# Performance work log

Measured on AMD Instinct MI355X. Metric: run time of the kernel, lower is better.

The kernel has to match this reference:

```python
import jax, jax.numpy as jnp
import numpy as np

B, S, HID = 2, 2048, 4096
NH, D = 32, 128          # heads, head_dim
G, GS = 8, 4             # palu groups, group_size (heads per group)
RK = 256                 # rank per K group (rank_k[i])
RV = 2048                # total V rank
FGD = RV // G            # fused_group_dim = 256
FH = FGD * NH            # fused_hidden_dim = 8192
GD = HID // G            # k group_dim = 512
THETA = 10000.0


def setup_inputs() -> dict:
    key = jax.random.key(0)
    ks = jax.random.split(key, 7)
    hidden_states = jax.random.normal(ks[0], (B, S, HID), jnp.float32)
    causal = jnp.tril(jnp.ones((S, S), bool))
    attention_mask = jnp.broadcast_to(
        jnp.where(causal, 0.0, -1e9).astype(jnp.float32)[None, None], (B, 1, S, S))
    position_ids = jnp.broadcast_to(jnp.arange(S, dtype=jnp.int32)[None], (B, S))
    sc = 0.02
    Wq = sc * jax.random.normal(ks[1], (HID, HID), jnp.float32)
    WVT = sc * jax.random.normal(ks[2], (G * RK, HID), jnp.float32)   # k_proj.VT
    U = sc * jax.random.normal(ks[3], (GD, G * RK), jnp.float32)      # k_proj.U
    Wv = sc * jax.random.normal(ks[4], (RV, HID), jnp.float32)
    Wo = sc * jax.random.normal(ks[5], (HID, FH), jnp.float32)
    return dict(hidden_states=hidden_states, attention_mask=attention_mask,
                position_ids=position_ids, Wq=Wq, WVT=WVT, U=U, Wv=Wv, Wo=Wo)


def _rotate_half(x):
    return jnp.concatenate([-x[..., D // 2:], x[..., :D // 2]], axis=-1)


def reference(hidden_states, attention_mask, position_ids, Wq, WVT, U, Wv, Wo):
    b, q, _ = hidden_states.shape
    # projections
    qs = (hidden_states @ Wq.T).reshape(b, q, NH, D).transpose(0, 2, 1, 3)      # (b,H,q,d)
    k_lat = (hidden_states @ WVT.T).reshape(b, q, G, RK).transpose(0, 2, 1, 3)  # (b,G,q,RK)
    v_lat = (hidden_states @ Wv.T).reshape(b, q, G, FGD).transpose(0, 2, 1, 3)  # (b,G,q,FGD)
    # headwise reconstruction of K: group g latent (RK) -> group_dim (512) via U[:, g-slice]
    Ug = U.reshape(GD, G, RK)
    keys = jnp.einsum('bgsr,dgr->bgsd', k_lat, Ug)                 # (b,G,q,512)
    keys = keys.transpose(0, 2, 1, 3).reshape(b, q, NH, D).transpose(0, 2, 1, 3)  # (b,H,q,d)
    # RoPE
    inv_freq = 1.0 / (THETA ** (jnp.arange(0, D, 2, dtype=jnp.float32) / D))
    freqs = position_ids.astype(jnp.float32)[..., None] * inv_freq            # (b,q,d/2)
    emb = jnp.concatenate([freqs, freqs], axis=-1)
    cos, sin = jnp.cos(emb)[:, None], jnp.sin(emb)[:, None]                   # (b,1,q,d)
    qs = qs * cos + _rotate_half(qs) * sin
    keys = keys * cos + _rotate_half(keys) * sin
    # attention scores + mask + fp32 softmax
    attn = jnp.einsum('bhqd,bhkd->bhqk', qs, keys) / np.sqrt(D).astype(np.float32)
    attn = attn + attention_mask
    attn = jax.nn.softmax(attn.astype(jnp.float32), axis=-1).astype(qs.dtype)
    # PALU fused low-rank V path: exact torch reshape/transpose semantics
    aw = attn.reshape(b, G, q * GS, q)                                        # (b,G,gs*q,kv)
    out = jnp.einsum('bgik,bgkf->bgif', aw, v_lat)                            # (b,G,gs*q,FGD)
    out = out.transpose(0, 2, 1, 3).reshape(b, q, FH)                         # (b,q,8192)
    return out @ Wo.T
```

## Files before the change

kernel.cpp:

```cpp
#include <hip/hip_runtime.h>
#include <hip/hip_bf16.h>

typedef __hip_bfloat16 bf16;
typedef __bf16 bf16x8 __attribute__((ext_vector_type(8)));
typedef float f32x4 __attribute__((ext_vector_type(4)));

#define MFMA16(a, b, c) __builtin_amdgcn_mfma_f32_16x16x32_bf16(a, b, c, 0, 0, 0)

__device__ __forceinline__ void llds16(const bf16* g, bf16* lds) {
  __builtin_amdgcn_global_load_lds(
      (const __attribute__((address_space(1))) unsigned int*)g,
      (__attribute__((address_space(3))) unsigned int*)lds, 16, 0, 0);
}

__device__ __forceinline__ void storeC(float* p, float v) { *p = v; }
__device__ __forceinline__ void storeC(bf16* p, float v) { *p = __float2bfloat16(v); }

__global__ __launch_bounds__(256) void cvt_f2b(const float* __restrict__ in,
                                               bf16* __restrict__ out, int n4) {
  int i = blockIdx.x * 256 + threadIdx.x;
  if (i >= n4) return;
  float4 v = ((const float4*)in)[i];
  union { bf16 h[4]; short4 s; } u;
  u.h[0] = __float2bfloat16(v.x);
  u.h[1] = __float2bfloat16(v.y);
  u.h[2] = __float2bfloat16(v.z);
  u.h[3] = __float2bfloat16(v.w);
  ((short4*)out)[i] = u.s;
}

template <typename OUT_T>
__global__ __launch_bounds__(512, 2) void gemm256(
    const bf16* __restrict__ A, const bf16* __restrict__ B, OUT_T* __restrict__ C,
    int K, int lda, int ldb, int ldc) {
  extern __shared__ bf16 sm[];
  const int t = threadIdx.x, w = t >> 6, l = t & 63;
  const int lane_r = l & 15, quad = l >> 4;
  const int wm = (w >> 2) * 128, wn = (w & 3) * 64;
  const long m0 = (long)blockIdx.y * 256, n0 = (long)blockIdx.x * 256;
  const int r0 = t >> 2;
  const int c0 = (((t & 3) ^ (r0 & 3)) << 3);
  const bf16* As0 = A + (m0 + r0) * lda + c0;
  const bf16* As1 = A + (m0 + r0 + 128) * lda + c0;
  const bf16* Bs0 = B + (n0 + r0) * ldb + c0;
  const bf16* Bs1 = B + (n0 + r0 + 128) * ldb + c0;

#define STAGE(sl, kt)                                   \
  do {                                                  \
    long ko = (long)(kt) * 32;                          \
    bf16* dA = sm + (sl) * 16384;                       \
    bf16* dB = dA + 8192;                               \
    llds16(As0 + ko, dA + t * 8);                       \
    llds16(As1 + ko, dA + (t + 512) * 8);               \
    llds16(Bs0 + ko, dB + t * 8);                       \
    llds16(Bs1 + ko, dB + (t + 512) * 8);               \
  } while (0)

  f32x4 acc[8][4] = {};
  const int KT = K >> 5;
  const int sw = quad ^ (lane_r & 3);

  STAGE(0, 0);
  STAGE(1, 1);
  int sl = 0;
  for (int kt = 0; kt < KT; ++kt) {
    const int pre = KT - 1 - kt;
    if (pre >= 2) {
      int sl2 = sl + 2;
      if (sl2 >= 3) sl2 -= 3;
      STAGE(sl2, kt + 2);
      asm volatile("s_waitcnt vmcnt(8)" ::: "memory");
    } else if (pre == 1) {
      asm volatile("s_waitcnt vmcnt(4)" ::: "memory");
    } else {
      asm volatile("s_waitcnt vmcnt(0)" ::: "memory");
    }
    __builtin_amdgcn_s_barrier();
    __builtin_amdgcn_sched_barrier(0);
    const bf16* Al = sm + sl * 16384;
    const bf16* Bl = Al + 8192;
    bf16x8 af[8], bfr[4];
#pragma unroll
    for (int mt = 0; mt < 8; ++mt)
      af[mt] = *(const bf16x8*)&Al[(wm + mt * 16 + lane_r) * 32 + sw * 8];
#pragma unroll
    for (int nt = 0; nt < 4; ++nt)
      bfr[nt] = *(const bf16x8*)&Bl[(wn + nt * 16 + lane_r) * 32 + sw * 8];
    __builtin_amdgcn_s_setprio(1);
#pragma unroll
    for (int mt = 0; mt < 8; ++mt)
#pragma unroll
      for (int nt = 0; nt < 4; ++nt)
        acc[mt][nt] = MFMA16(af[mt], bfr[nt], acc[mt][nt]);
    __builtin_amdgcn_s_setprio(0);
    __builtin_amdgcn_s_barrier();
    if (++sl == 3) sl = 0;
  }
#undef STAGE

#pragma unroll
  for (int mt = 0; mt < 8; ++mt)
#pragma unroll
    for (int nt = 0; nt < 4; ++nt) {
      long row = m0 + wm + mt * 16 + quad * 4;
      long col = n0 + wn + nt * 16 + lane_r;
#pragma unroll
      for (int r = 0; r < 4; ++r) storeC(&C[(row + r) * ldc + col], acc[mt][nt][r]);
    }
}

template <typename OUT_T>
__global__ __launch_bounds__(256) void gemm_bt(
    const bf16* __restrict__ A, const bf16* __restrict__ B, OUT_T* __restrict__ C,
    int M, int N, int K, int lda, int ldb, int ldc,
    long batchA, long batchB, long batchC) {
  __shared__ alignas(16) bf16 As[128 * 32];
  __shared__ alignas(16) bf16 Bs[128 * 32];
  const int t = threadIdx.x;
  const int w = t >> 6, l = t & 63;
  const int lane_r = l & 15, quad = l >> 4;
  const int wm = (w >> 1) * 64, wn = (w & 1) * 64;
  const long m0 = (long)blockIdx.y * 128, n0 = (long)blockIdx.x * 128;
  A += (long)blockIdx.z * batchA;
  B += (long)blockIdx.z * batchB;
  C += (long)blockIdx.z * batchC;
  const int r0a = t >> 2;
  const int cba = (t & 3) * 8;
  f32x4 acc[4][4] = {};
  for (int k0 = 0; k0 < K; k0 += 32) {
    llds16(A + (m0 + r0a) * lda + k0 + cba, &As[t * 8]);
    llds16(A + (m0 + r0a + 64) * lda + k0 + cba, &As[(t + 256) * 8]);
    llds16(B + (n0 + r0a) * ldb + k0 + cba, &Bs[t * 8]);
    llds16(B + (n0 + r0a + 64) * ldb + k0 + cba, &Bs[(t + 256) * 8]);
    __syncthreads();
    bf16x8 af[4], bfr[4];
#pragma unroll
    for (int mt = 0; mt < 4; ++mt)
      af[mt] = *(const bf16x8*)&As[(wm + mt * 16 + lane_r) * 32 + quad * 8];
#pragma unroll
    for (int nt = 0; nt < 4; ++nt)
      bfr[nt] = *(const bf16x8*)&Bs[(wn + nt * 16 + lane_r) * 32 + quad * 8];
#pragma unroll
    for (int mt = 0; mt < 4; ++mt)
#pragma unroll
      for (int nt = 0; nt < 4; ++nt)
        acc[mt][nt] = MFMA16(af[mt], bfr[nt], acc[mt][nt]);
    __syncthreads();
  }
#pragma unroll
  for (int mt = 0; mt < 4; ++mt)
#pragma unroll
    for (int nt = 0; nt < 4; ++nt) {
      long row = m0 + wm + mt * 16 + quad * 4;
      long col = n0 + wn + nt * 16 + lane_r;
#pragma unroll
      for (int r = 0; r < 4; ++r) storeC(&C[(row + r) * ldc + col], acc[mt][nt][r]);
    }
}

__global__ __launch_bounds__(256) void rope_perm(const bf16* __restrict__ in, int ldin,
                                                 bf16* __restrict__ out,
                                                 const int* __restrict__ pos_ids) {
  int idx = blockIdx.x * 256 + threadIdx.x;
  int d = idx & 63;
  int h = (idx >> 6) & 31;
  int bs = idx >> 11;
  int b = bs >> 11, s = bs & 2047;
  float pos = (float)pos_ids[bs];
  float inv = exp2f(-(float)d * (13.287712379549449f / 64.0f));
  float fr = pos * inv, sn, cs;
  sincosf(fr, &sn, &cs);
  long bi = (long)bs * ldin + h * 128 + d;
  long bo = ((long)(b * 32 + h) * 2048 + s) * 128 + d;
  float x1 = __bfloat162float(in[bi]);
  float x2 = __bfloat162float(in[bi + 64]);
  out[bo] = __float2bfloat16(x1 * cs - x2 * sn);
  out[bo + 64] = __float2bfloat16(x2 * cs + x1 * sn);
}

__global__ __launch_bounds__(256) void transpose_kernel(const bf16* __restrict__ v,
                                                        int ldv,
                                                        bf16* __restrict__ vt) {
  __shared__ bf16 tile[32][33];
  int b = blockIdx.z;
  int c0 = blockIdx.x * 32;
  int r0 = blockIdx.y * 32;
  int tx = threadIdx.x & 31, ty = threadIdx.x >> 5;
#pragma unroll
  for (int p = 0; p < 4; ++p) {
    int r = ty + p * 8;
    tile[r][tx] = v[((long)b * 2048 + r0 + r) * ldv + c0 + tx];
  }
  __syncthreads();
#pragma unroll
  for (int p = 0; p < 4; ++p) {
    int cidx = ty + p * 8;
    int cg = c0 + cidx;
    int g = cg >> 8, d = cg & 255;
    int s = r0 + tx;
    vt[((long)((b * 8 + g) * 64 + (s >> 5))) * 8192 + d * 32 + (s & 31)] = tile[tx][cidx];
  }
}

__global__ __launch_bounds__(512, 2) void attn_kernel(const bf16* __restrict__ Q,
                                                      const bf16* __restrict__ Kg,
                                                      const bf16* __restrict__ Vt,
                                                      bf16* __restrict__ fused) {
  __shared__ alignas(16) bf16 smem[32768];
  const int t = threadIdx.x, w = t >> 6, l = t & 63;
  const int lane_r = l & 15, quad = l >> 4;
  const int L = blockIdx.x;
  const int half = L >> 8, pair = L & 255;
  const int hb = pair >> 2, slot = pair & 3;
  const int qt = half ? slot : (7 - slot);
  const int b = hb >> 5, h = hb & 31;
  const int g = h >> 2, j = h & 3;
  const int q0 = qt * 256;
  const int qr0 = q0 + w * 32;
  const float scale = 0.08838834764831845f;

  const bf16* qbase = Q + ((long)(b * 32 + h) * 2048 + qr0 + lane_r) * 128 + quad * 8;
  bf16x8 qf[2][4];
#pragma unroll
  for (int m = 0; m < 2; ++m)
#pragma unroll
    for (int kd = 0; kd < 4; ++kd)
      qf[m][kd] = *(const bf16x8*)(qbase + m * 2048 + kd * 32);

  f32x4 acc[2][16] = {};
  float m_i[2][4], l_i[2][4];
#pragma unroll
  for (int m = 0; m < 2; ++m)
#pragma unroll
    for (int r = 0; r < 4; ++r) { m_i[m][r] = -1e30f; l_i[m][r] = 0.f; }

  const bf16* Kf = Kg + (long)(b * 32 + h) * 262144 + lane_r * 128 + quad * 8;
  const bf16* Vf = Vt + (long)(b * 8 + g) * 524288 + lane_r * 32 + quad * 8;
  bf16* Pw = smem + w * 1024;
  const int pslot = quad ^ ((lane_r >> 1) & 3);
  int poff0[4], poff1[4];
  {
    const int hi = lane_r >> 3, lo = lane_r & 7;
#pragma unroll
    for (int r = 0; r < 4; ++r) {
      int rq = quad * 4 + r;
      int sw = (rq >> 1) & 3;
      poff0[r] = rq * 32 + ((hi ^ sw) << 3) + lo;
      poff1[r] = rq * 32 + (((2 + hi) ^ sw) << 3) + lo;
    }
  }

  const int nkw = (qr0 >> 5) + 1;
  for (int kt = 0; kt < nkw; ++kt) {
    const int k0 = kt * 32;
    const bool diag = (kt == nkw - 1);
    const bf16* Kt_ = Kf + (long)k0 * 128;
    const bf16* Vt_ = Vf + (long)kt * 8192;

    f32x4 s[2][2] = {};
#pragma unroll
    for (int ks = 0; ks < 2; ++ks) {
      bf16x8 kf[4];
#pragma unroll
      for (int kd = 0; kd < 4; ++kd)
        kf[kd] = *(const bf16x8*)(Kt_ + ks * 2048 + kd * 32);
#pragma unroll
      for (int kd = 0; kd < 4; ++kd) {
        s[0][ks] = MFMA16(qf[0][kd], kf[kd], s[0][ks]);
        s[1][ks] = MFMA16(qf[1][kd], kf[kd], s[1][ks]);
      }
    }
    float sc[2][2][4];
    if (diag) {
#pragma unroll
      for (int m = 0; m < 2; ++m) {
        const int qrowb = qr0 + m * 16 + quad * 4;
#pragma unroll
        for (int r = 0; r < 4; ++r) {
          sc[m][0][r] = (k0 + lane_r <= qrowb + r) ? s[m][0][r] * scale : -1e30f;
          sc[m][1][r] = (k0 + 16 + lane_r <= qrowb + r) ? s[m][1][r] * scale : -1e30f;
        }
      }
    } else {
#pragma unroll
      for (int m = 0; m < 2; ++m)
#pragma unroll
        for (int r = 0; r < 4; ++r) {
          sc[m][0][r] = s[m][0][r] * scale;
          sc[m][1][r] = s[m][1][r] * scale;
        }
    }

#pragma unroll
    for (int m = 0; m < 2; ++m) {
      float mx[4];
      bool grow = false;
#pragma unroll
      for (int r = 0; r < 4; ++r) {
        float v = fmaxf(sc[m][0][r], sc[m][1][r]);
#pragma unroll
        for (int o = 1; o < 16; o <<= 1) v = fmaxf(v, __shfl_xor(v, o));
        mx[r] = v;
        grow = grow || (v > m_i[m][r]);
      }
      if (__any((int)grow)) {
#pragma unroll
        for (int r = 0; r < 4; ++r) {
          float mnew = fmaxf(m_i[m][r], mx[r]);
          float alpha = __expf(m_i[m][r] - mnew);
          m_i[m][r] = mnew;
          l_i[m][r] *= alpha;
#pragma unroll
          for (int nt = 0; nt < 16; ++nt) acc[m][nt][r] *= alpha;
        }
      }
#pragma unroll
      for (int r = 0; r < 4; ++r) {
        float p0 = __expf(sc[m][0][r] - m_i[m][r]);
        float p1 = __expf(sc[m][1][r] - m_i[m][r]);
        float rs = p0 + p1;
#pragma unroll
        for (int o = 1; o < 16; o <<= 1) rs += __shfl_xor(rs, o);
        l_i[m][r] += rs;
        Pw[m * 512 + poff0[r]] = __float2bfloat16(p0);
        Pw[m * 512 + poff1[r]] = __float2bfloat16(p1);
      }
    }

    bf16x8 pf0 = *(const bf16x8*)&Pw[lane_r * 32 + pslot * 8];
    bf16x8 pf1 = *(const bf16x8*)&Pw[(16 + lane_r) * 32 + pslot * 8];
    __builtin_amdgcn_s_setprio(1);
#pragma unroll
    for (int nt = 0; nt < 16; ++nt) {
      bf16x8 vf = *(const bf16x8*)(Vt_ + nt * 512);
      acc[0][nt] = MFMA16(pf0, vf, acc[0][nt]);
      acc[1][nt] = MFMA16(pf1, vf, acc[1][nt]);
    }
    __builtin_amdgcn_s_setprio(0);
  }

  __syncthreads();
  bf16* EP = smem + w * 4096;
#pragma unroll
  for (int m = 0; m < 2; ++m) {
#pragma unroll
    for (int r = 0; r < 4; ++r) {
      float inv = 1.0f / l_i[m][r];
#pragma unroll
      for (int nt = 0; nt < 16; ++nt)
        EP[(quad * 4 + r) * 256 + nt * 16 + lane_r] = __float2bfloat16(acc[m][nt][r] * inv);
    }
#pragma unroll
    for (int op = 0; op < 8; ++op) {
      int row = op * 2 + (l >> 5);
      int qrow = qr0 + m * 16 + row;
      int sOut = j * 512 + (qrow >> 2), fi = qrow & 3;
      bf16x8 vread = *(const bf16x8*)&EP[row * 256 + (l & 31) * 8];
      *(bf16x8*)(fused + ((long)(b * 2048 + sOut)) * 8192 + fi * 2048 + g * 256 +
                 (l & 31) * 8) = vread;
    }
  }
}

extern "C" void kernel_launch(void* const* d_in, const int* in_sizes, int n_in,
                              void* d_out, int out_size, void* d_ws, size_t ws_size,
                              hipStream_t stream) {
  const float* hidden = (const float*)d_in[0];
  const int* pos_ids = (const int*)d_in[2];
  const float* Wq = (const float*)d_in[3];
  const float* WVT = (const float*)d_in[4];
  const float* U = (const float*)d_in[5];
  const float* Wv = (const float*)d_in[6];
  const float* Wo = (const float*)d_in[7];
  float* out = (float*)d_out;

  bf16* ws = (bf16*)d_ws;
  bf16* WB = ws;
  bf16* UB = WB + 33554432;
  bf16* hidB = UB + 1048576;
  bf16* proj = hidB + 16777216;
  bf16* Kb = proj + 33554432;
  bf16* vtB = Kb + 16777216;
  bf16* fusedB = vtB + 8388608;
  bf16* Qh = hidB;
  bf16* Kh = proj;

  static bool attr_set = false;
  if (!attr_set) {
    hipFuncSetAttribute((const void*)gemm256<bf16>,
                        hipFuncAttributeMaxDynamicSharedMemorySize, 98304);
    hipFuncSetAttribute((const void*)gemm256<float>,
                        hipFuncAttributeMaxDynamicSharedMemorySize, 98304);
    attr_set = true;
  }

  cvt_f2b<<<16384, 256, 0, stream>>>(hidden, hidB, 4194304);
  cvt_f2b<<<16384, 256, 0, stream>>>(Wq, WB, 4194304);
  cvt_f2b<<<8192, 256, 0, stream>>>(WVT, WB + 16777216, 2097152);
  cvt_f2b<<<8192, 256, 0, stream>>>(Wv, WB + 25165824, 2097152);
  gemm256<bf16><<<dim3(32, 16), 512, 98304, stream>>>(hidB, WB, proj, 4096, 4096,
                                                      4096, 8192);
  cvt_f2b<<<1024, 256, 0, stream>>>(U, UB, 262144);
  gemm_bt<bf16><<<dim3(4, 32, 8), 256, 0, stream>>>(proj + 4096, UB, Kb, 4096, 512,
                                                    256, 8192, 2048, 4096, 256, 256,
                                                    512);
  transpose_kernel<<<dim3(64, 64, 2), 256, 0, stream>>>(proj + 6144, 8192, vtB);
  rope_perm<<<32768, 256, 0, stream>>>(proj, 8192, Qh, pos_ids);
  rope_perm<<<32768, 256, 0, stream>>>(Kb, 4096, Kh, pos_ids);
  cvt_f2b<<<32768, 256, 0, stream>>>(Wo, WB, 8388608);
  attn_kernel<<<dim3(512, 1, 1), 512, 0, stream>>>(Qh, Kh, vtB, fusedB);
  gemm256<float><<<dim3(16, 16), 512, 98304, stream>>>(fusedB, WB, out, 8192, 8192,
                                                       8192, 4096);
}
```

Measured before the change: 1.383 ms.

## Stage K/V tiles in LDS with double-buffered async loads shared across waves

The attention kernel previously had each wave read K and V fragments directly from global memory. It now cooperatively loads each 32-key K tile and its V tile into swizzled LDS using global_load_lds, double-buffered so the next tile's fetch overlaps the current tile's compute. All waves in the block share the staged tiles, which cuts redundant global traffic. Waves past their causal limit skip the compute but still take part in loads and barriers, which adds two barriers per tile plus extra LDS use that may lower occupancy.

```diff
diff --git a/kernel.cpp b/kernel.cpp
--- a/kernel.cpp
+++ b/kernel.cpp
@@ -234,110 +234,143 @@
 #pragma unroll
     for (int r = 0; r < 4; ++r) { m_i[m][r] = -1e30f; l_i[m][r] = 0.f; }
 
-  const bf16* Kf = Kg + (long)(b * 32 + h) * 262144 + lane_r * 128 + quad * 8;
-  const bf16* Vf = Vt + (long)(b * 8 + g) * 524288 + lane_r * 32 + quad * 8;
-  bf16* Pw = smem + w * 1024;
+  const bf16* Kbase = Kg + (long)(b * 32 + h) * 262144;
+  const bf16* Vtg = Vt + (long)(b * 8 + g) * 524288;
+  const int kr = t >> 4, ck = (t & 15) ^ (kr & 15);
+  const bf16* ksrc = Kbase + kr * 128 + ck * 8;
+  const int vrA = t >> 2, cvA = (t & 3) ^ (vrA & 3);
+  const int vrB = (t + 512) >> 2, cvB = ((t + 512) & 3) ^ (vrB & 3);
+  const bf16* vsrcA = Vtg + vrA * 32 + cvA * 8;
+  const bf16* vsrcB = Vtg + vrB * 32 + cvB * 8;
+
+#define STAGE_T(buf, kt)                                                    \
+  do {                                                                      \
+    llds16(ksrc + (long)(kt) * 4096, &smem[(buf) * 4096 + t * 8]);          \
+    llds16(vsrcA + (long)(kt) * 8192, &smem[8192 + (buf) * 8192 + t * 8]);  \
+    llds16(vsrcB + (long)(kt) * 8192,                                       \
+           &smem[8192 + (buf) * 8192 + (t + 512) * 8]);                     \
+  } while (0)
+
+  bf16* Pw = smem + 24576 + w * 1024;
   const int pslot = quad ^ ((lane_r >> 1) & 3);
+  const int vslot = quad ^ (lane_r & 3);
   int poff0[4], poff1[4];
   {
     const int hi = lane_r >> 3, lo = lane_r & 7;
 #pragma unroll
     for (int r = 0; r < 4; ++r) {
       int rq = quad * 4 + r;
-      int sw = (rq >> 1) & 3;
-      poff0[r] = rq * 32 + ((hi ^ sw) << 3) + lo;
-      poff1[r] = rq * 32 + (((2 + hi) ^ sw) << 3) + lo;
-    }
-  }
-
-  const int nkw = (qr0 >> 5) + 1;
-  for (int kt = 0; kt < nkw; ++kt) {
-    const int k0 = kt * 32;
-    const bool diag = (kt == nkw - 1);
-    const bf16* Kt_ = Kf + (long)k0 * 128;
-    const bf16* Vt_ = Vf + (long)kt * 8192;
-
-    f32x4 s[2][2] = {};
-#pragma unroll
-    for (int ks = 0; ks < 2; ++ks) {
-      bf16x8 kf[4];
-#pragma unroll
-      for (int kd = 0; kd < 4; ++kd)
-        kf[kd] = *(const bf16x8*)(Kt_ + ks * 2048 + kd * 32);
-#pragma unroll
-      for (int kd = 0; kd < 4; ++kd) {
-        s[0][ks] = MFMA16(qf[0][kd], kf[kd], s[0][ks]);
-        s[1][ks] = MFMA16(qf[1][kd], kf[kd], s[1][ks]);
+      int sw2 = (rq >> 1) & 3;
+      poff0[r] = rq * 32 + ((hi ^ sw2) << 3) + lo;
+      poff1[r] = rq * 32 + (((2 + hi) ^ sw2) << 3) + lo;
+    }
+  }
+
+  const int nk = qt * 8 + 8;
+  const int kwmax = qt * 8 + w;
+
+  STAGE_T(0, 0);
+  for (int kt = 0; kt < nk; ++kt) {
+    if (kt + 1 < nk) {
+      STAGE_T((kt + 1) & 1, kt + 1);
+      asm volatile("s_waitcnt vmcnt(3)" ::: "memory");
+    } else {
+      asm volatile("s_waitcnt vmcnt(0)" ::: "memory");
+    }
+    __builtin_amdgcn_s_barrier();
+    __builtin_amdgcn_sched_barrier(0);
+    const bf16* Ks = &smem[(kt & 1) * 4096];
+    const bf16* Vs = &smem[8192 + (kt & 1) * 8192];
+
+    if (kt <= kwmax) {
+      const int k0 = kt * 32;
+      const bool diag = (kt == kwmax);
+      f32x4 s[2][2] = {};
+#pragma unroll
+      for (int ks = 0; ks < 2; ++ks) {
+        bf16x8 kf[4];
+#pragma unroll
+        for (int kd = 0; kd < 4; ++kd) {
+          int csw = (kd * 4 + quad) ^ lane_r;
+          kf[kd] = *(const bf16x8*)&Ks[(ks * 16 + lane_r) * 128 + csw * 8];
+        }
+#pragma unroll
+        for (int kd = 0; kd < 4; ++kd) {
+          s[0][ks] = MFMA16(qf[0][kd], kf[kd], s[0][ks]);
+          s[1][ks] = MFMA16(qf[1][kd], kf[kd], s[1][ks]);
+        }
       }
-    }
-    float sc[2][2][4];
-    if (diag) {
+      float sc[2][2][4];
+      if (diag) {
+#pragma unroll
+        for (int m = 0; m < 2; ++m) {
+          const int qrowb = qr0 + m * 16 + quad * 4;
+#pragma unroll
+          for (int r = 0; r < 4; ++r) {
+            sc[m][0][r] = (k0 + lane_r <= qrowb + r) ? s[m][0][r] * scale : -1e30f;
+            sc[m][1][r] = (k0 + 16 + lane_r <= qrowb + r) ? s[m][1][r] * scale : -1e30f;
+          }
+        }
+      } else {
+#pragma unroll
+        for (int m = 0; m < 2; ++m)
+#pragma unroll
+          for (int r = 0; r < 4; ++r) {
+            sc[m][0][r] = s[m][0][r] * scale;
+            sc[m][1][r] = s[m][1][r] * scale;
+          }
+      }
+
 #pragma unroll
       for (int m = 0; m < 2; ++m) {
-        const int qrowb = qr0 + m * 16 + quad * 4;
+        float mx[4];
+        bool grow = false;
 #pragma unroll
         for (int r = 0; r < 4; ++r) {
-          sc[m][0][r] = (k0 + lane_r <= qrowb + r) ? s[m][0][r] * scale : -1e30f;
-          sc[m][1][r] = (k0 + 16 + lane_r <= qrowb + r) ? s[m][1][r] * scale : -1e30f;
+          float v = fmaxf(sc[m][0][r], sc[m][1][r]);
+#pragma unroll
+          for (int o = 1; o < 16; o <<= 1) v = fmaxf(v, __shfl_xor(v, o));
+          mx[r] = v;
+          grow = grow || (v > m_i[m][r]);
+        }
+        if (__any((int)grow)) {
+#pragma unroll
+          for (int r = 0; r < 4; ++r) {
+            float mnew = fmaxf(m_i[m][r], mx[r]);
+            float alpha = __expf(m_i[m][r] - mnew);
+            m_i[m][r] = mnew;
+            l_i[m][r] *= alpha;
+#pragma unroll
+            for (int nt = 0; nt < 16; ++nt) acc[m][nt][r] *= alpha;
+          }
+        }
+#pragma unroll
+        for (int r = 0; r < 4; ++r) {
+          float p0 = __expf(sc[m][0][r] - m_i[m][r]);
+          float p1 = __expf(sc[m][1][r] - m_i[m][r]);
+          float rs = p0 + p1;
+#pragma unroll
+          for (int o = 1; o < 16; o <<= 1) rs += __shfl_xor(rs, o);
+          l_i[m][r] += rs;
+          Pw[m * 512 + poff0[r]] = __float2bfloat16(p0);
+          Pw[m * 512 + poff1[r]] = __float2bfloat16(p1);
         }
       }
-    } else {
-#pragma unroll
-      for (int m = 0; m < 2; ++m)
-#pragma unroll
-        for (int r = 0; r < 4; ++r) {
-          sc[m][0][r] = s[m][0][r] * scale;
-          sc[m][1][r] = s[m][1][r] * scale;
-        }
-    }
-
-#pragma unroll
-    for (int m = 0; m < 2; ++m) {
-      float mx[4];
-      bool grow = false;
-#pragma unroll
-      for (int r = 0; r < 4; ++r) {
-        float v = fmaxf(sc[m][0][r], sc[m][1][r]);
-#pragma unroll
-        for (int o = 1; o < 16; o <<= 1) v = fmaxf(v, __shfl_xor(v, o));
-        mx[r] = v;
-        grow = grow || (v > m_i[m][r]);
+
+      bf16x8 pf0 = *(const bf16x8*)&Pw[lane_r * 32 + pslot * 8];
+      bf16x8 pf1 = *(const bf16x8*)&Pw[(16 + lane_r) * 32 + pslot * 8];
+      __builtin_amdgcn_s_setprio(1);
+#pragma unroll
+      for (int nt = 0; nt < 16; ++nt) {
+        bf16x8 vf = *(const bf16x8*)&Vs[(nt * 16 + lane_r) * 32 + vslot * 8];
+        acc[0][nt] = MFMA16(pf0, vf, acc[0][nt]);
+        acc[1][nt] = MFMA16(pf1, vf, acc[1][nt]);
       }
-      if (__any((int)grow)) {
-#pragma unroll
-        for (int r = 0; r < 4; ++r) {
-          float mnew = fmaxf(m_i[m][r], mx[r]);
-          float alpha = __expf(m_i[m][r] - mnew);
-          m_i[m][r] = mnew;
-          l_i[m][r] *= alpha;
-#pragma unroll
-          for (int nt = 0; nt < 16; ++nt) acc[m][nt][r] *= alpha;
-        }
-      }
-#pragma unroll
-      for (int r = 0; r < 4; ++r) {
-        float p0 = __expf(sc[m][0][r] - m_i[m][r]);
-        float p1 = __expf(sc[m][1][r] - m_i[m][r]);
-        float rs = p0 + p1;
-#pragma unroll
-        for (int o = 1; o < 16; o <<= 1) rs += __shfl_xor(rs, o);
-        l_i[m][r] += rs;
-        Pw[m * 512 + poff0[r]] = __float2bfloat16(p0);
-        Pw[m * 512 + poff1[r]] = __float2bfloat16(p1);
-      }
-    }
-
-    bf16x8 pf0 = *(const bf16x8*)&Pw[lane_r * 32 + pslot * 8];
-    bf16x8 pf1 = *(const bf16x8*)&Pw[(16 + lane_r) * 32 + pslot * 8];
-    __builtin_amdgcn_s_setprio(1);
-#pragma unroll
-    for (int nt = 0; nt < 16; ++nt) {
-      bf16x8 vf = *(const bf16x8*)(Vt_ + nt * 512);
-      acc[0][nt] = MFMA16(pf0, vf, acc[0][nt]);
-      acc[1][nt] = MFMA16(pf1, vf, acc[1][nt]);
-    }
-    __builtin_amdgcn_s_setprio(0);
-  }
+      __builtin_amdgcn_s_setprio(0);
+    }
+    __builtin_amdgcn_s_barrier();
+  }
+#undef STAGE_T
 
   __syncthreads();
   bf16* EP = smem + w * 4096;
```

Result: faster. 1.193 ms (-13.8%).
